# Performance work log

Hardware: AMD Instinct MI355X
Metric: run time of the kernel (lower is better)

Reference implementation:

```python
import jax, jax.numpy as jnp
import numpy as np

L, B, D, NB = 2048, 8, 128, 16  # seq_len, inner batch, hidden=input size, num SRU instances


def setup_inputs() -> dict:
    key = jax.random.key(0)
    k1, k2, k3 = jax.random.split(key, 3)
    x = jax.random.normal(k1, (L, B, D, NB), dtype=jnp.float32)
    # per-instance SRU weights: projections for x_tilde, forget gate, reset gate
    W = jax.random.normal(k2, (NB, D, 3 * D), dtype=jnp.float32) * (1.0 / np.sqrt(D))
    # per-instance biases for forget and reset gates
    b = jax.random.normal(k3, (NB, 2 * D), dtype=jnp.float32) * 0.1
    return {"x": x, "W": W, "b": b}


def _batch_sru(x, W, b):
    # x: (L, B, D, NB) -> move instance axis next to batch: (L, B, NB, D)
    xt = jnp.moveaxis(x, -1, 2)
    # one fused GEMM over all instances instead of a Python loop per SRU
    U = jnp.einsum('lbkd,kdh->lbkh', xt, W)  # (L, B, NB, 3D)
    x_tilde, f_pre, r_pre = jnp.split(U, 3, axis=-1)
    bf, br = jnp.split(b, 2, axis=-1)  # each (NB, D), broadcasts over (L, B)
    f = jax.nn.sigmoid(f_pre + bf)
    r = jax.nn.sigmoid(r_pre + br)

    def step(c, inp):
        x_t, f_t = inp
        c = f_t * c + (1.0 - f_t) * x_t  # elementwise linear recurrence
        return c, c

    c0 = jnp.zeros(x_tilde.shape[1:], x_tilde.dtype)  # (B, NB, D)
    _, cs = jax.lax.scan(step, c0, (x_tilde, f))  # cs: (L, B, NB, D)
    h = r * cs + (1.0 - r) * xt  # highway connection (needs input==hidden size)
    return jnp.moveaxis(h, 2, -1)  # back to (L, B, D, NB), stacked on dim=-1


def reference(x, W, b):
    return _batch_sru(x, W, b)
```

## Files before the change

### kernel.cpp

```cpp
#include <hip/hip_runtime.h>


typedef float f32x4 __attribute__((ext_vector_type(4)));
typedef _Float16 f16x8 __attribute__((ext_vector_type(8)));
typedef unsigned int u32;
typedef u32 u32x4 __attribute__((ext_vector_type(4)));
typedef unsigned short u16;

__device__ inline u32 pack_hl(float x) {
  _Float16 h = (_Float16)x;
  _Float16 l = (_Float16)(x - (float)h);
  u32 uh = (u32)__builtin_bit_cast(u16, h);
  u32 ul = (u32)__builtin_bit_cast(u16, l);
  return uh | (ul << 16);
}
__device__ inline float unpack_hl(u32 v) {
  return (float)__builtin_bit_cast(_Float16, (u16)(v & 0xffffu)) +
         (float)__builtin_bit_cast(_Float16, (u16)(v >> 16));
}

__global__ __launch_bounds__(256) void k_wprep(const float* __restrict__ W,
                                               _Float16* __restrict__ Wfh,
                                               _Float16* __restrict__ Wfl) {
  int e = blockIdx.x * 256 + threadIdx.x;
  int lam = e & 63;
  int t = e >> 6;
  int s = t & 3; t >>= 2;
  int w = t & 7; t >>= 3;
  int cti = t % 3;
  int k = t / 3;
  const float* Wp = W + (size_t)k * 128 * 384 + (size_t)(cti * 128 + 16 * w + (lam & 15));
  int row0 = 32 * s + 8 * (lam >> 4);
  size_t o = (size_t)e * 8;
#pragma unroll
  for (int ii = 0; ii < 8; ++ii) {
    float v = Wp[(size_t)(row0 + ii) * 384];
    _Float16 h = (_Float16)v;
    Wfh[o + ii] = h;
    Wfl[o + ii] = (_Float16)(v - (float)h);
  }
}

__global__ __launch_bounds__(256) void k_prep(const float* __restrict__ x,
                                              u32* __restrict__ XP) {
  __shared__ u32 S[2][16 * 193];
  const int bid = blockIdx.x;
  const int b = bid & 7, l0 = (bid >> 3) * 4;
  const int t = threadIdx.x;
  const int d0 = t >> 1, kc = t & 1;
  const int kk = t >> 4, dc = t & 15;
  const int pw = d0 + 4 * (d0 >> 3);
  for (int li = 0; li < 4; ++li) {
    const int l = l0 + li;
    const float* src = x + ((size_t)(l * 8 + b) * 128 + d0) * 16 + kc * 8;
    f32x4 v0 = *(const f32x4*)src;
    f32x4 v1 = *(const f32x4*)(src + 4);
    u32* Sw = S[li & 1];
#pragma unroll
    for (int i = 0; i < 8; ++i) {
      float xv = (i < 4) ? v0[i] : v1[i - 4];
      Sw[(kc * 8 + i) * 193 + pw] = pack_hl(xv);
    }
    __syncthreads();
    u32 vv[8];
#pragma unroll
    for (int e = 0; e < 8; ++e) vv[e] = Sw[kk * 193 + 12 * dc + e];
    size_t o = ((size_t)(kk * 8 + b) * 2048 + l) * 128 + dc * 8;
    *(u32x4*)(XP + o) = (u32x4){vv[0], vv[1], vv[2], vv[3]};
    *(u32x4*)(XP + o + 4) = (u32x4){vv[4], vv[5], vv[6], vv[7]};
  }
}

__global__ __launch_bounds__(640) void k_sru(
    u32* __restrict__ XP, const _Float16* __restrict__ Wfh,
    const _Float16* __restrict__ Wfl, const float* __restrict__ bias,
    _Float16* __restrict__ rP, float* __restrict__ Pseg,
    float* __restrict__ Cend) {
  __shared__ u32 Xp[3][16 * 128];
  __shared__ u32 Ut[2][16 * 320];

  const int bid = blockIdx.x;
  const int b = bid & 7, k = (bid >> 3) & 15, s = bid >> 7;
  const int tid = threadIdx.x, wl = tid & 63, w = tid >> 6;
  const size_t chanbase = (size_t)(k * 8 + b);
  const size_t rowbase = chanbase * 2048 + (size_t)s * 256;

  f16x8 BH[3][4], BL[3][4];
  float biasF = 0.f, biasR = 0.f;
  if (w < 8) {
#pragma unroll
    for (int cti = 0; cti < 3; ++cti)
#pragma unroll
      for (int s2 = 0; s2 < 4; ++s2) {
        size_t off = ((((size_t)(k * 3 + cti) * 8 + w) * 4 + s2) * 64 + wl) * 8;
        BH[cti][s2] = *(const f16x8*)(Wfh + off);
        BL[cti][s2] = *(const f16x8*)(Wfl + off);
      }
    int cx = 16 * w + (wl & 15);
    biasF = bias[k * 256 + cx];
    biasR = bias[k * 256 + 128 + cx];
  }

  auto stage = [&](int tile) {
    int nb = tile % 3;
    int r = 2 * w + (wl >> 5);
    int a = wl & 31;
    int cslot = a >> 1;
    int clog = cslot ^ (r & 7);
    int within = (a & 1) * 4;
    const u32* src = XP + (rowbase + tile * 16 + r) * 128 + clog * 8 + within;
    __builtin_amdgcn_global_load_lds(
        (const __attribute__((address_space(1))) void*)src,
        (__attribute__((address_space(3))) void*)&Xp[nb][2 * w * 128], 16, 0, 0);
  };

  auto gemm = [&](int tile) {
    const int nb = tile % 3, ub = tile & 1;
    const int n = wl & 15, g = wl >> 4;
    f32x4 a0 = {0.f, 0.f, 0.f, 0.f}, a1 = a0, a2 = a0;
#pragma unroll
    for (int s2 = 0; s2 < 4; ++s2) {
      int slot = (4 * s2 + g) ^ (n & 7);
      const u32* px = &Xp[nb][n * 128 + slot * 8];
      u32x4 q0 = *(const u32x4*)px;
      u32x4 q1 = *(const u32x4*)(px + 4);
      u32 h0 = __builtin_amdgcn_perm(q0[1], q0[0], 0x05040100u);
      u32 h1 = __builtin_amdgcn_perm(q0[3], q0[2], 0x05040100u);
      u32 h2 = __builtin_amdgcn_perm(q1[1], q1[0], 0x05040100u);
      u32 h3 = __builtin_amdgcn_perm(q1[3], q1[2], 0x05040100u);
      u32 l0 = __builtin_amdgcn_perm(q0[1], q0[0], 0x07060302u);
      u32 l1 = __builtin_amdgcn_perm(q0[3], q0[2], 0x07060302u);
      u32 l2 = __builtin_amdgcn_perm(q1[1], q1[0], 0x07060302u);
      u32 l3 = __builtin_amdgcn_perm(q1[3], q1[2], 0x07060302u);
      f16x8 ah = __builtin_bit_cast(f16x8, (u32x4){h0, h1, h2, h3});
      f16x8 al = __builtin_bit_cast(f16x8, (u32x4){l0, l1, l2, l3});
      a0 = __builtin_amdgcn_mfma_f32_16x16x32_f16(ah, BH[0][s2], a0, 0, 0, 0);
      a1 = __builtin_amdgcn_mfma_f32_16x16x32_f16(ah, BH[1][s2], a1, 0, 0, 0);
      a2 = __builtin_amdgcn_mfma_f32_16x16x32_f16(ah, BH[2][s2], a2, 0, 0, 0);
      a0 = __builtin_amdgcn_mfma_f32_16x16x32_f16(al, BH[0][s2], a0, 0, 0, 0);
      a1 = __builtin_amdgcn_mfma_f32_16x16x32_f16(al, BH[1][s2], a1, 0, 0, 0);
      a2 = __builtin_amdgcn_mfma_f32_16x16x32_f16(al, BH[2][s2], a2, 0, 0, 0);
      a0 = __builtin_amdgcn_mfma_f32_16x16x32_f16(ah, BL[0][s2], a0, 0, 0, 0);
      a1 = __builtin_amdgcn_mfma_f32_16x16x32_f16(ah, BL[1][s2], a1, 0, 0, 0);
      a2 = __builtin_amdgcn_mfma_f32_16x16x32_f16(ah, BL[2][s2], a2, 0, 0, 0);
    }
    float* Uf = (float*)Ut[ub];
    _Float16* Uh = (_Float16*)Ut[ub];
    const int cx = 16 * w + n;
#pragma unroll
    for (int e = 0; e < 4; ++e) {
      int row = 4 * g + e;
      int rot = 4 * (row & 7);
      Uf[row * 320 + ((cx + rot) & 127)] = a0[e];
      float fv = 1.f / (1.f + __expf(-(a1[e] + biasF)));
      Uf[row * 320 + 128 + ((cx + rot) & 127)] = fv;
      float rv = 1.f / (1.f + __expf(-(a2[e] + biasR)));
      Uh[(row * 320 + 256 + (((cx >> 1) + rot) & 63)) * 2 + (cx & 1)] = (_Float16)rv;
    }
  };

  float c = 0.f, P = 1.f;

  auto scan = [&](int tile) {
    const int ub = tile & 1;
    const int d = (w - 8) * 64 + wl;
    const float* Uf = (const float*)Ut[ub];
    const _Float16* Uh = (const _Float16*)Ut[ub];
    const size_t growbase = (rowbase + tile * 16) * 128 + d;
    u32 xw[16];
#pragma unroll
    for (int m = 0; m < 16; ++m) xw[m] = XP[growbase + (size_t)m * 128];
    float* H0 = (float*)XP;
    const bool storeRP = tile < 4;
#pragma unroll
    for (int m = 0; m < 16; ++m) {
      int rot = 4 * (m & 7);
      float xt = Uf[m * 320 + ((d + rot) & 127)];
      float fv = Uf[m * 320 + 128 + ((d + rot) & 127)];
      float rv = (float)Uh[(m * 320 + 256 + (((d >> 1) + rot) & 63)) * 2 + (d & 1)];
      c = xt + fv * (c - xt);
      P *= fv;
      if (storeRP)
        rP[((chanbase * 8 + s) * 64 + (tile * 16 + m)) * 128 + d] = (_Float16)(rv * P);
      float xval = unpack_hl(xw[m]);
      H0[growbase + (size_t)m * 128] = xval + rv * (c - xval);
    }
  };

  if (w < 8) { stage(0); stage(1); }
  if (w < 8) asm volatile("s_waitcnt vmcnt(1) lgkmcnt(0)" ::: "memory");
  __builtin_amdgcn_s_barrier();
  __builtin_amdgcn_sched_barrier(0);

  for (int i = 0; i < 16; ++i) {
    if (w < 8) {
      if (i < 14) stage(i + 2);
      gemm(i);
    } else {
      if (i >= 1) scan(i - 1);
    }
    __builtin_amdgcn_sched_barrier(0);
    if (w < 8) {
      if (i < 14) asm volatile("s_waitcnt vmcnt(1) lgkmcnt(0)" ::: "memory");
      else        asm volatile("s_waitcnt vmcnt(0) lgkmcnt(0)" ::: "memory");
    }
    __builtin_amdgcn_s_barrier();
    __builtin_amdgcn_sched_barrier(0);
  }

  if (w >= 8) {
    scan(15);
    int d = (w - 8) * 64 + wl;
    size_t ch = chanbase * 128 + d;
    Pseg[(size_t)s * 16384 + ch] = P;
    Cend[(size_t)s * 16384 + ch] = c;
  }
}

__global__ __launch_bounds__(256) void k_comb(const float* __restrict__ Pseg,
                                              const float* __restrict__ Cend,
                                              float* __restrict__ Cin) {
  int ch = blockIdx.x * 256 + threadIdx.x;
  float c = 0.f;
#pragma unroll
  for (int s = 0; s < 8; ++s) {
    Cin[s * 16384 + ch] = c;
    c = Cend[s * 16384 + ch] + Pseg[s * 16384 + ch] * c;
  }
}

__global__ __launch_bounds__(256) void k_fin(const float* __restrict__ H0,
                                             const _Float16* __restrict__ rP,
                                             const float* __restrict__ Cin,
                                             float* __restrict__ out) {
  __shared__ float S[2][16 * 193];
  const int bid = blockIdx.x;
  const int b = bid & 7, l0 = (bid >> 3) * 4;
  const int t = threadIdx.x;
  const int kk = t >> 4, dc = t & 15;
  const int d0 = t >> 1, kc = t & 1;
  const int pw = d0 + 4 * (d0 >> 3);
  for (int li = 0; li < 4; ++li) {
    const int l = l0 + li;
    const int sseg = l >> 8, lloc = l & 255;
    size_t hb = ((size_t)(kk * 8 + b) * 2048 + l) * 128 + dc * 8;
    f32x4 h0a = *(const f32x4*)(H0 + hb);
    f32x4 h0b = *(const f32x4*)(H0 + hb + 4);
    if (lloc < 64) {
      size_t rb = (((size_t)(kk * 8 + b) * 8 + sseg) * 64 + lloc) * 128 + dc * 8;
      f16x8 rp8 = *(const f16x8*)(rP + rb);
      size_t cb = (size_t)sseg * 16384 + (size_t)(kk * 8 + b) * 128 + dc * 8;
      f32x4 c0 = *(const f32x4*)(Cin + cb);
      f32x4 c1 = *(const f32x4*)(Cin + cb + 4);
#pragma unroll
      for (int e = 0; e < 4; ++e) {
        h0a[e] += (float)rp8[e] * c0[e];
        h0b[e] += (float)rp8[4 + e] * c1[e];
      }
    }
    float* Sw = S[li & 1];
#pragma unroll
    for (int e = 0; e < 8; ++e)
      Sw[kk * 193 + 12 * dc + e] = (e < 4) ? h0a[e] : h0b[e - 4];
    __syncthreads();
    float ov[8];
#pragma unroll
    for (int i = 0; i < 8; ++i) ov[i] = Sw[(kc * 8 + i) * 193 + pw];
    size_t oo = ((size_t)(l * 8 + b) * 128 + d0) * 16 + kc * 8;
    *(f32x4*)(out + oo) = (f32x4){ov[0], ov[1], ov[2], ov[3]};
    *(f32x4*)(out + oo + 4) = (f32x4){ov[4], ov[5], ov[6], ov[7]};
  }
}

extern "C" void kernel_launch(void* const* d_in, const int* in_sizes, int n_in,
                              void* d_out, int out_size, void* d_ws, size_t ws_size,
                              hipStream_t stream) {
  (void)in_sizes; (void)n_in; (void)out_size; (void)ws_size;
  const float* x = (const float*)d_in[0];
  const float* W = (const float*)d_in[1];
  const float* bias = (const float*)d_in[2];
  float* out = (float*)d_out;
  char* ws = (char*)d_ws;
  u32* XP        = (u32*)ws;
  _Float16* Wfh  = (_Float16*)(ws + 134217728);
  _Float16* Wfl  = (_Float16*)(ws + 135790592);
  _Float16* rPp  = (_Float16*)(ws + 137363456);
  float* Pseg    = (float*)(ws + 154140672);
  float* Cend    = (float*)(ws + 154664960);
  float* Cin     = (float*)(ws + 155189248);

  k_wprep<<<384, 256, 0, stream>>>(W, Wfh, Wfl);
  k_prep<<<4096, 256, 0, stream>>>(x, XP);
  k_sru<<<1024, 640, 0, stream>>>(XP, Wfh, Wfl, bias, rPp, Pseg, Cend);
  k_comb<<<64, 256, 0, stream>>>(Pseg, Cend, Cin);
  k_fin<<<4096, 256, 0, stream>>>((const float*)XP, rPp, Cin, out);
}
```

Before: 437.8 us.

## Fuse scan into GEMM waves with in-register parallel scan and direct output writes

Removes the producer/consumer split between GEMM waves and scan waves. Each GEMM wave now runs a shuffle-based parallel prefix scan over its 16-row MFMA tile and writes h directly into the final (L,B,D,NB) output layout. The old full-size H0 round trip through workspace and the transposing finalize kernel are replaced by a small fix-up kernel that only adds the carry-in term to the first 64 rows of each segment. In exchange, the output writes are strided and uncoalesced (stride 16 across k) and X is loaded straight from global memory without LDS staging. Launch shape also changes to 256-thread blocks with an XCD-aware block mapping.

```diff
diff --git a/kernel.cpp b/kernel.cpp
--- a/kernel.cpp
+++ b/kernel.cpp
@@ -71,59 +71,55 @@
   }
 }
 
-__global__ __launch_bounds__(640) void k_sru(
-    u32* __restrict__ XP, const _Float16* __restrict__ Wfh,
+__global__ __launch_bounds__(256, 3) void k_sru(
+    const u32* __restrict__ XP, const _Float16* __restrict__ Wfh,
     const _Float16* __restrict__ Wfl, const float* __restrict__ bias,
-    _Float16* __restrict__ rP, float* __restrict__ Pseg,
-    float* __restrict__ Cend) {
-  __shared__ u32 Xp[3][16 * 128];
-  __shared__ u32 Ut[2][16 * 320];
-
+    float* __restrict__ out, _Float16* __restrict__ rP,
+    float* __restrict__ Pseg, float* __restrict__ Cend) {
   const int bid = blockIdx.x;
-  const int b = bid & 7, k = (bid >> 3) & 15, s = bid >> 7;
-  const int tid = threadIdx.x, wl = tid & 63, w = tid >> 6;
-  const size_t chanbase = (size_t)(k * 8 + b);
-  const size_t rowbase = chanbase * 2048 + (size_t)s * 256;
+  const int xcd = bid & 7, idx = bid >> 3;
+  const int grp = xcd * 8 + (idx >> 5);
+  const int sub = idx & 31;
+  const int b = grp & 7, seg = grp >> 3;
+  const int k = sub >> 1, half = sub & 1;
+  const int tid = threadIdx.x, wl = tid & 63;
+  const int wcol = half * 4 + (tid >> 6);
+  const int n = wl & 15, g = wl >> 4;
+  const int col = 16 * wcol + n;
 
   f16x8 BH[3][4], BL[3][4];
-  float biasF = 0.f, biasR = 0.f;
-  if (w < 8) {
-#pragma unroll
-    for (int cti = 0; cti < 3; ++cti)
-#pragma unroll
-      for (int s2 = 0; s2 < 4; ++s2) {
-        size_t off = ((((size_t)(k * 3 + cti) * 8 + w) * 4 + s2) * 64 + wl) * 8;
-        BH[cti][s2] = *(const f16x8*)(Wfh + off);
-        BL[cti][s2] = *(const f16x8*)(Wfl + off);
-      }
-    int cx = 16 * w + (wl & 15);
-    biasF = bias[k * 256 + cx];
-    biasR = bias[k * 256 + 128 + cx];
-  }
-
-  auto stage = [&](int tile) {
-    int nb = tile % 3;
-    int r = 2 * w + (wl >> 5);
-    int a = wl & 31;
-    int cslot = a >> 1;
-    int clog = cslot ^ (r & 7);
-    int within = (a & 1) * 4;
-    const u32* src = XP + (rowbase + tile * 16 + r) * 128 + clog * 8 + within;
-    __builtin_amdgcn_global_load_lds(
-        (const __attribute__((address_space(1))) void*)src,
-        (__attribute__((address_space(3))) void*)&Xp[nb][2 * w * 128], 16, 0, 0);
-  };
-
-  auto gemm = [&](int tile) {
-    const int nb = tile % 3, ub = tile & 1;
-    const int n = wl & 15, g = wl >> 4;
+#pragma unroll
+  for (int cti = 0; cti < 3; ++cti)
+#pragma unroll
+    for (int s2 = 0; s2 < 4; ++s2) {
+      size_t off = ((((size_t)(k * 3 + cti) * 8 + wcol) * 4 + s2) * 64 + wl) * 8;
+      BH[cti][s2] = *(const f16x8*)(Wfh + off);
+      BL[cti][s2] = *(const f16x8*)(Wfl + off);
+    }
+  const float biasF = bias[k * 256 + col];
+  const float biasR = bias[k * 256 + 128 + col];
+
+  const u32* Xbase = XP + ((size_t)(k * 8 + b) * 2048 + (size_t)seg * 256) * 128;
+
+  float cseg = 0.f, carryP = 1.f;
+
+  for (int t = 0; t < 16; ++t) {
+    u32x4 q[8];
+#pragma unroll
+    for (int s2 = 0; s2 < 4; ++s2) {
+      const u32* p = Xbase + (size_t)(t * 16 + n) * 128 + 32 * s2 + 8 * g;
+      q[2 * s2] = *(const u32x4*)p;
+      q[2 * s2 + 1] = *(const u32x4*)(p + 4);
+    }
+    float xv[4];
+#pragma unroll
+    for (int e = 0; e < 4; ++e)
+      xv[e] = unpack_hl(Xbase[(size_t)(t * 16 + 4 * g + e) * 128 + col]);
+
     f32x4 a0 = {0.f, 0.f, 0.f, 0.f}, a1 = a0, a2 = a0;
 #pragma unroll
     for (int s2 = 0; s2 < 4; ++s2) {
-      int slot = (4 * s2 + g) ^ (n & 7);
-      const u32* px = &Xp[nb][n * 128 + slot * 8];
-      u32x4 q0 = *(const u32x4*)px;
-      u32x4 q1 = *(const u32x4*)(px + 4);
+      u32x4 q0 = q[2 * s2], q1 = q[2 * s2 + 1];
       u32 h0 = __builtin_amdgcn_perm(q0[1], q0[0], 0x05040100u);
       u32 h1 = __builtin_amdgcn_perm(q0[3], q0[2], 0x05040100u);
       u32 h2 = __builtin_amdgcn_perm(q1[1], q1[0], 0x05040100u);
@@ -144,76 +140,57 @@
       a1 = __builtin_amdgcn_mfma_f32_16x16x32_f16(ah, BL[1][s2], a1, 0, 0, 0);
       a2 = __builtin_amdgcn_mfma_f32_16x16x32_f16(ah, BL[2][s2], a2, 0, 0, 0);
     }
-    float* Uf = (float*)Ut[ub];
-    _Float16* Uh = (_Float16*)Ut[ub];
-    const int cx = 16 * w + n;
+
+    float f[4], r[4];
 #pragma unroll
     for (int e = 0; e < 4; ++e) {
-      int row = 4 * g + e;
-      int rot = 4 * (row & 7);
-      Uf[row * 320 + ((cx + rot) & 127)] = a0[e];
-      float fv = 1.f / (1.f + __expf(-(a1[e] + biasF)));
-      Uf[row * 320 + 128 + ((cx + rot) & 127)] = fv;
-      float rv = 1.f / (1.f + __expf(-(a2[e] + biasR)));
-      Uh[(row * 320 + 256 + (((cx >> 1) + rot) & 63)) * 2 + (cx & 1)] = (_Float16)rv;
-    }
-  };
-
-  float c = 0.f, P = 1.f;
-
-  auto scan = [&](int tile) {
-    const int ub = tile & 1;
-    const int d = (w - 8) * 64 + wl;
-    const float* Uf = (const float*)Ut[ub];
-    const _Float16* Uh = (const _Float16*)Ut[ub];
-    const size_t growbase = (rowbase + tile * 16) * 128 + d;
-    u32 xw[16];
-#pragma unroll
-    for (int m = 0; m < 16; ++m) xw[m] = XP[growbase + (size_t)m * 128];
-    float* H0 = (float*)XP;
-    const bool storeRP = tile < 4;
-#pragma unroll
-    for (int m = 0; m < 16; ++m) {
-      int rot = 4 * (m & 7);
-      float xt = Uf[m * 320 + ((d + rot) & 127)];
-      float fv = Uf[m * 320 + 128 + ((d + rot) & 127)];
-      float rv = (float)Uh[(m * 320 + 256 + (((d >> 1) + rot) & 63)) * 2 + (d & 1)];
-      c = xt + fv * (c - xt);
-      P *= fv;
-      if (storeRP)
-        rP[((chanbase * 8 + s) * 64 + (tile * 16 + m)) * 128 + d] = (_Float16)(rv * P);
-      float xval = unpack_hl(xw[m]);
-      H0[growbase + (size_t)m * 128] = xval + rv * (c - xval);
-    }
-  };
-
-  if (w < 8) { stage(0); stage(1); }
-  if (w < 8) asm volatile("s_waitcnt vmcnt(1) lgkmcnt(0)" ::: "memory");
-  __builtin_amdgcn_s_barrier();
-  __builtin_amdgcn_sched_barrier(0);
-
-  for (int i = 0; i < 16; ++i) {
-    if (w < 8) {
-      if (i < 14) stage(i + 2);
-      gemm(i);
-    } else {
-      if (i >= 1) scan(i - 1);
-    }
-    __builtin_amdgcn_sched_barrier(0);
-    if (w < 8) {
-      if (i < 14) asm volatile("s_waitcnt vmcnt(1) lgkmcnt(0)" ::: "memory");
-      else        asm volatile("s_waitcnt vmcnt(0) lgkmcnt(0)" ::: "memory");
-    }
-    __builtin_amdgcn_s_barrier();
-    __builtin_amdgcn_sched_barrier(0);
-  }
-
-  if (w >= 8) {
-    scan(15);
-    int d = (w - 8) * 64 + wl;
-    size_t ch = chanbase * 128 + d;
-    Pseg[(size_t)s * 16384 + ch] = P;
-    Cend[(size_t)s * 16384 + ch] = c;
+      f[e] = 1.f / (1.f + __expf(-(a1[e] + biasF)));
+      r[e] = 1.f / (1.f + __expf(-(a2[e] + biasR)));
+    }
+
+    float Pl = f[0] * f[1] * f[2] * f[3];
+    float Cl = 0.f;
+#pragma unroll
+    for (int e = 0; e < 4; ++e) Cl = f[e] * Cl + (1.f - f[e]) * a0[e];
+
+    float Pi = Pl, Ci = Cl;
+    {
+      float Pp = __shfl(Pi, wl - 16);
+      float Cp = __shfl(Ci, wl - 16);
+      if (g >= 1) { Ci = Ci + Pi * Cp; Pi = Pi * Pp; }
+    }
+    {
+      float Pp = __shfl(Pi, wl - 32);
+      float Cp = __shfl(Ci, wl - 32);
+      if (g >= 2) { Ci = Ci + Pi * Cp; Pi = Pi * Pp; }
+    }
+    float Pe = __shfl(Pi, wl - 16);
+    float Ce = __shfl(Ci, wl - 16);
+    if (g == 0) { Pe = 1.f; Ce = 0.f; }
+    float c = Ce + Pe * cseg;
+    float p = carryP * Pe;
+    float Pall = __shfl(Pi, n + 48);
+    float Call = __shfl(Ci, n + 48);
+    cseg = Call + Pall * cseg;
+    carryP = carryP * Pall;
+
+#pragma unroll
+    for (int e = 0; e < 4; ++e) {
+      c = f[e] * c + (1.f - f[e]) * a0[e];
+      p = p * f[e];
+      float h = xv[e] + r[e] * (c - xv[e]);
+      int row = t * 16 + 4 * g + e;
+      out[((size_t)((seg * 256 + row) * 8 + b)) * 2048 + col * 16 + k] = h;
+      if (t < 4)
+        rP[((((size_t)(b * 8 + seg) * 64) + row) * 128 + col) * 16 + k] =
+            (_Float16)(r[e] * p);
+    }
+  }
+
+  if (g == 0) {
+    size_t o = (size_t)seg * 16384 + (size_t)(k * 8 + b) * 128 + col;
+    Pseg[o] = carryP;
+    Cend[o] = cseg;
   }
 }
 
@@ -229,46 +206,35 @@
   }
 }
 
-__global__ __launch_bounds__(256) void k_fin(const float* __restrict__ H0,
+__global__ __launch_bounds__(256) void k_fix(float* __restrict__ out,
                                              const _Float16* __restrict__ rP,
-                                             const float* __restrict__ Cin,
-                                             float* __restrict__ out) {
-  __shared__ float S[2][16 * 193];
+                                             const float* __restrict__ Cin) {
   const int bid = blockIdx.x;
-  const int b = bid & 7, l0 = (bid >> 3) * 4;
-  const int t = threadIdx.x;
-  const int kk = t >> 4, dc = t & 15;
-  const int d0 = t >> 1, kc = t & 1;
-  const int pw = d0 + 4 * (d0 >> 3);
-  for (int li = 0; li < 4; ++li) {
-    const int l = l0 + li;
-    const int sseg = l >> 8, lloc = l & 255;
-    size_t hb = ((size_t)(kk * 8 + b) * 2048 + l) * 128 + dc * 8;
-    f32x4 h0a = *(const f32x4*)(H0 + hb);
-    f32x4 h0b = *(const f32x4*)(H0 + hb + 4);
-    if (lloc < 64) {
-      size_t rb = (((size_t)(kk * 8 + b) * 8 + sseg) * 64 + lloc) * 128 + dc * 8;
-      f16x8 rp8 = *(const f16x8*)(rP + rb);
-      size_t cb = (size_t)sseg * 16384 + (size_t)(kk * 8 + b) * 128 + dc * 8;
-      f32x4 c0 = *(const f32x4*)(Cin + cb);
-      f32x4 c1 = *(const f32x4*)(Cin + cb + 4);
-#pragma unroll
-      for (int e = 0; e < 4; ++e) {
-        h0a[e] += (float)rp8[e] * c0[e];
-        h0b[e] += (float)rp8[4 + e] * c1[e];
-      }
-    }
-    float* Sw = S[li & 1];
-#pragma unroll
-    for (int e = 0; e < 8; ++e)
-      Sw[kk * 193 + 12 * dc + e] = (e < 4) ? h0a[e] : h0b[e - 4];
-    __syncthreads();
-    float ov[8];
-#pragma unroll
-    for (int i = 0; i < 8; ++i) ov[i] = Sw[(kc * 8 + i) * 193 + pw];
-    size_t oo = ((size_t)(l * 8 + b) * 128 + d0) * 16 + kc * 8;
-    *(f32x4*)(out + oo) = (f32x4){ov[0], ov[1], ov[2], ov[3]};
-    *(f32x4*)(out + oo + 4) = (f32x4){ov[4], ov[5], ov[6], ov[7]};
+  const int grp = bid >> 4, q = bid & 15;
+  const int b = grp & 7, seg = grp >> 3;
+  const int tid = threadIdx.x;
+  __shared__ float Cs[2048];
+  for (int i = tid; i < 2048; i += 256) {
+    int kk = i >> 7, d = i & 127;
+    Cs[i] = Cin[(size_t)seg * 16384 + (size_t)(kk * 8 + b) * 128 + d];
+  }
+  __syncthreads();
+  const int d = tid >> 1, kh = (tid & 1) * 8;
+  for (int rr = 0; rr < 4; ++rr) {
+    int row = q * 4 + rr;
+    size_t ob = ((size_t)((seg * 256 + row) * 8 + b)) * 2048 + d * 16 + kh;
+    f32x4 o0 = *(f32x4*)(out + ob);
+    f32x4 o1 = *(f32x4*)(out + ob + 4);
+    const _Float16* rp =
+        rP + ((((size_t)(b * 8 + seg) * 64) + row) * 128 + d) * 16 + kh;
+    f16x8 rv = *(const f16x8*)rp;
+#pragma unroll
+    for (int e = 0; e < 4; ++e) {
+      o0[e] += (float)rv[e] * Cs[(kh + e) * 128 + d];
+      o1[e] += (float)rv[4 + e] * Cs[(kh + 4 + e) * 128 + d];
+    }
+    *(f32x4*)(out + ob) = o0;
+    *(f32x4*)(out + ob + 4) = o1;
   }
 }
 
@@ -291,7 +257,7 @@
 
   k_wprep<<<384, 256, 0, stream>>>(W, Wfh, Wfl);
   k_prep<<<4096, 256, 0, stream>>>(x, XP);
-  k_sru<<<1024, 640, 0, stream>>>(XP, Wfh, Wfl, bias, rPp, Pseg, Cend);
+  k_sru<<<2048, 256, 0, stream>>>(XP, Wfh, Wfl, bias, out, rPp, Pseg, Cend);
   k_comb<<<64, 256, 0, stream>>>(Pseg, Cend, Cin);
-  k_fin<<<4096, 256, 0, stream>>>((const float*)XP, rPp, Cin, out);
-}
+  k_fix<<<1024, 256, 0, stream>>>(out, rPp, Cin);
+}
```

Measured after the change: 544.4 us. 24.3% more time.
